# Optimization experiments

Measured on AMD Instinct MI355X. Metric: run time of the kernel, lower is better.

Reference implementation:

```python
import jax, jax.numpy as jnp
import numpy as np

B, S, D, H, G, K = 4, 4096, 1024, 16, 4, 3
DG = D // G   # group channels = 256
DH = D // H   # head channels = 64


def setup_inputs() -> dict:
    key = jax.random.key(0)
    ks = jax.random.split(key, 8)
    def w(k, shape, std=0.02):
        return jax.random.normal(k, shape, jnp.float32) * std
    return {
        "x": jax.random.normal(ks[0], (B, S, D), jnp.float32),
        "Wq": w(ks[1], (D, D)), "bq": jnp.zeros((D,), jnp.float32),
        "Wk": w(ks[2], (D, D)), "bk": jnp.zeros((D,), jnp.float32),
        "Wv": w(ks[3], (D, D)), "bv": jnp.zeros((D,), jnp.float32),
        "Wo": w(ks[4], (D, D)), "bo": jnp.zeros((D,), jnp.float32),
        "Woff1": w(ks[5], (DG, DG, K)), "boff1": jnp.zeros((DG,), jnp.float32),
        "Woff2": w(ks[6], (DG,)),
        "bias_table": w(ks[7], (1, 1, S)),
    }


def reference(x, Wq, bq, Wk, bk, Wv, bv, Wo, bo, Woff1, boff1, Woff2, bias_table):
    bsz, seq, d = x.shape
    scale = d ** (-0.5)
    xc = jnp.transpose(x, (0, 2, 1))  # [B, D, S]

    # 1x1 conv projections == channel GEMMs
    q = jnp.einsum('oc,bcs->bos', Wq, xc) + bq[None, :, None]  # [B, D, S]

    # group: [B*G, DG, S]
    gq = q.reshape(bsz * G, DG, seq)
    # offset head: conv1d(k=3, pad=1) -> conv1d(k=1, no bias) -> [B*G, S]
    h = jax.lax.conv_general_dilated(
        gq, Woff1, window_strides=(1,), padding=((K // 2, K // 2),),
        dimension_numbers=('NCH', 'OIH', 'NCH')) + boff1[None, :, None]
    offset = jnp.einsum('c,bcs->bs', Woff2, h)
    offset = jnp.tanh(offset) * K  # offset_range_factor = kernel

    gx = xc.reshape(bsz * G, DG, seq)  # grouped x

    # faithful replication of _grid_sample_1d: F.grid_sample on feats [N,C,S,1]
    # with grid (x = vgrid_scaled -> width dim of size 1, y = 0 -> height dim of
    # size S), bilinear, zero padding, align_corners=False.
    grid = jnp.arange(seq, dtype=x.dtype)[None, :]
    vgrid_scaled = 2.0 * (grid + offset) / max(seq - 1, 1) - 1.0  # [B*G, S]
    ix = vgrid_scaled / 2.0                 # unnormalized width coord (W=1)
    wx = jnp.clip(1.0 - jnp.abs(ix), 0.0, 1.0)  # bilinear weight on width idx 0
    iy = (seq - 1) / 2.0                    # unnormalized height coord for y=0
    y0 = int(np.floor(iy)); y1 = min(y0 + 1, seq - 1)
    wy1 = float(iy - y0); wy0 = 1.0 - wy1
    feat_c = wy0 * gx[:, :, y0] + wy1 * gx[:, :, y1]  # [B*G, DG]
    x_sampled = feat_c[:, :, None] * wx[:, None, :]   # [B*G, DG, S]
    xs = x_sampled.reshape(bsz, d, seq)               # ungroup -> [B, D, S]

    k = jnp.einsum('oc,bcs->bos', Wk, xs) + bk[None, :, None]
    v = jnp.einsum('oc,bcs->bos', Wv, xs) + bv[None, :, None]

    qh = q.reshape(bsz * H, DH, seq)
    kh = k.reshape(bsz * H, DH, seq)
    vh = v.reshape(bsz * H, DH, seq) + bias_table[:, :, :seq]

    # channel attention: contract over sequence dim (as in the original einsum)
    scores = jnp.einsum('bis,bjs->bij', qh, kh) * scale  # [B*H, DH, DH]
    attn = jax.nn.softmax(scores, axis=-1)
    out = jnp.einsum('bij,bjs->bis', attn, vh)           # [B*H, DH, S]
    out = out.reshape(bsz, d, seq).transpose(0, 2, 1)     # [B, S, D]
    return jnp.einsum('bsd,od->bso', out, Wo) + bo
```

## Files before the change

kernel.cpp:

```cpp
#include <hip/hip_runtime.h>
#include <math.h>

#define BB 4
#define SS 4096
#define DD 1024
#define HH 16
#define GG 4
#define KK 3
#define DG 256
#define DH 64
#define CH 16
#define NCH (SS / CH)

enum : size_t {
  OFF_WEFF  = 0,
  OFF_OFFC  = 1024,
  OFF_WEQ   = 1280,
  OFF_ZT    = 13568,
  OFF_WX    = 210176,
  OFF_XWP   = 275712,
  OFF_XW    = 5518592,
  OFF_XS    = 5534976,
  OFF_SW    = 5539072,
  OFF_FEAT  = 5539328,
  OFF_KF    = 5543424,
  OFF_VF    = 5559808,
  OFF_AV    = 5576192,
  OFF_AB    = 5592576,
  OFF_C2    = 5596672,
  OFF_WAV   = 5600768,
  OFF_WOSUM = 5617152,
  WS_FLOATS = 5618176
};

__device__ __forceinline__ float wred_sum(float v) {
#pragma unroll
  for (int o = 32; o > 0; o >>= 1) v += __shfl_xor(v, o, 64);
  return v;
}
__device__ __forceinline__ float wred_max(float v) {
#pragma unroll
  for (int o = 32; o > 0; o >>= 1) v = fmaxf(v, __shfl_xor(v, o, 64));
  return v;
}

__global__ void k_pre1(const float* __restrict__ Woff1, const float* __restrict__ Woff2,
                       const float* __restrict__ x, const float* __restrict__ Wo,
                       float* __restrict__ ws) {
  const int t = threadIdx.x;
  const int lane = t & 63;
  if (blockIdx.x < 192) {
    const int widx = (blockIdx.x * 256 + t) >> 6;
    const int i = widx / 3, kk = widx - 3 * i;
    float a = 0.f;
#pragma unroll
    for (int u = 0; u < 4; ++u) {
      const int cc = lane + 64 * u;
      a += Woff2[cc] * Woff1[(size_t)(cc * DG + i) * KK + kk];
    }
    a = wred_sum(a);
    if (lane == 0) ws[OFF_WEFF + widx] = a;
  } else if (blockIdx.x < 208) {
    const int gid = (blockIdx.x - 192) * 256 + t;
    const int b = gid >> 10, c = gid & 1023;
    ws[OFF_FEAT + gid] = 0.5f * (x[((size_t)b * SS + 2047) * DD + c] +
                                 x[((size_t)b * SS + 2048) * DD + c]);
  } else {
    const int o = ((blockIdx.x - 208) * 256 + t) >> 6;
    const float4* wo = (const float4*)(Wo + (size_t)o * DD);
    float v = 0.f;
#pragma unroll
    for (int it = 0; it < 4; ++it) {
      const float4 a = wo[lane + 64 * it];
      v += a.x + a.y + a.z + a.w;
    }
    v = wred_sum(v);
    if (lane == 0) ws[OFF_WOSUM + o] = v;
  }
}

__global__ void k_pre2(const float* __restrict__ Wq, const float* __restrict__ bq,
                       const float* __restrict__ Woff2, const float* __restrict__ boff1,
                       const float* __restrict__ Wk, const float* __restrict__ Wv,
                       float* __restrict__ ws) {
  const float* Weff = ws + OFF_WEFF;
  const int t = threadIdx.x;
  const int lane = t & 63;
  if (blockIdx.x < 192) {
    const int j = blockIdx.x >> 4;
    const int c0 = (blockIdx.x & 15) * 64;
    const int g = j / 3, kk = j - 3 * g;
    const int q = t >> 6;
    float a = 0.f;
#pragma unroll 4
    for (int ii = 0; ii < 64; ++ii) {
      const int i = q * 64 + ii;
      a += Weff[i * KK + kk] * Wq[(size_t)(g * DG + i) * DD + c0 + lane];
    }
    __shared__ float red[4][64];
    red[q][lane] = a;
    __syncthreads();
    if (q == 0) {
      const float v = red[0][lane] + red[1][lane] + red[2][lane] + red[3][lane];
      ws[OFF_WEQ + (size_t)j * DD + c0 + lane] = v;
    }
  } else if (blockIdx.x == 192) {
    if (t >= 64) return;
    float beff = 0.f;
#pragma unroll
    for (int u = 0; u < 4; ++u) {
      const int cc = lane + 64 * u;
      beff += Woff2[cc] * boff1[cc];
    }
    beff = wred_sum(beff);
#pragma unroll
    for (int g = 0; g < 4; ++g) {
      float a = 0.f;
#pragma unroll
      for (int u = 0; u < 4; ++u) {
        const int i = lane + 64 * u;
        a += (Weff[i * 3 + 0] + Weff[i * 3 + 1] + Weff[i * 3 + 2]) * bq[g * DG + i];
      }
      a = wred_sum(a);
      if (lane == 0) ws[OFF_OFFC + g] = a + beff;
    }
  } else {
    const int widx = (blockIdx.x - 193) * 4 + (t >> 6);
    const int g = widx >> 10, o = widx & 1023;
    const float4 ak = ((const float4*)(Wk + (size_t)o * DD + g * DG))[lane];
    const float4 avv = ((const float4*)(Wv + (size_t)o * DD + g * DG))[lane];
    float kk[4], vv[4];
#pragma unroll
    for (int b = 0; b < 4; ++b) {
      const float4 f = ((const float4*)(ws + OFF_FEAT + (size_t)b * DD + g * DG))[lane];
      kk[b] = ak.x * f.x + ak.y * f.y + ak.z * f.z + ak.w * f.w;
      vv[b] = avv.x * f.x + avv.y * f.y + avv.z * f.z + avv.w * f.w;
    }
#pragma unroll
    for (int b = 0; b < 4; ++b) { kk[b] = wred_sum(kk[b]); vv[b] = wred_sum(vv[b]); }
    if (lane == 0) {
#pragma unroll
      for (int b = 0; b < 4; ++b) {
        ws[OFF_KF + ((size_t)(b * GG + g)) * DD + o] = kk[b];
        ws[OFF_VF + ((size_t)(b * GG + g)) * DD + o] = vv[b];
      }
    }
  }
}

__global__ __launch_bounds__(256, 2) void k_z(const float* __restrict__ x,
                                              const float* __restrict__ weq,
                                              float* __restrict__ zt) {
  const int lane = threadIdx.x & 63;
  const int wave = (blockIdx.x * blockDim.x + threadIdx.x) >> 6;
  const int nwaves = (gridDim.x * blockDim.x) >> 6;
  float4 w[12][4];
#pragma unroll
  for (int j = 0; j < 12; ++j)
#pragma unroll
    for (int it = 0; it < 4; ++it)
      w[j][it] = *(const float4*)(weq + (size_t)j * DD + 4 * (lane + 64 * it));
  for (int row = wave; row < BB * SS; row += nwaves) {
    const float4* xr = (const float4*)(x + (size_t)row * DD);
    float4 xv[4];
#pragma unroll
    for (int it = 0; it < 4; ++it) xv[it] = xr[lane + 64 * it];
    float acc[12];
#pragma unroll
    for (int j = 0; j < 12; ++j) {
      float a = 0.f;
#pragma unroll
      for (int it = 0; it < 4; ++it)
        a += xv[it].x * w[j][it].x + xv[it].y * w[j][it].y +
             xv[it].z * w[j][it].z + xv[it].w * w[j][it].w;
      acc[j] = a;
    }
#pragma unroll
    for (int j = 0; j < 12; ++j) acc[j] = wred_sum(acc[j]);
    if (lane == 0) {
#pragma unroll
      for (int j = 0; j < 12; ++j) zt[(size_t)row * 12 + j] = acc[j];
    }
  }
}

__global__ __launch_bounds__(256) void k_xw(const float* __restrict__ x,
                                            float* __restrict__ ws) {
  const int b = blockIdx.x >> 8;
  const int chunk = blockIdx.x & 255;
  const int s0 = chunk * CH;
  const int t = threadIdx.x;
  __shared__ float wxs[4][CH];

  if (t < 64) {
    const int g = t >> 4, si = t & 15;
    const int s = s0 + si;
    const size_t row = (size_t)b * SS + s;
    const float* zt = ws + OFF_ZT;
    float off = ws[OFF_OFFC + g];
    if (s > 0)      off += zt[(row - 1) * 12 + g * 3 + 0];
    off += zt[row * 12 + g * 3 + 1];
    if (s < SS - 1) off += zt[(row + 1) * 12 + g * 3 + 2];
    off = tanhf(off) * (float)KK;
    const float vg = 2.0f * ((float)s + off) / (float)(SS - 1) - 1.0f;
    float wvv = 1.0f - fabsf(0.5f * vg);
    wvv = fminf(fmaxf(wvv, 0.0f), 1.0f);
    wxs[g][si] = wvv;
    ws[OFF_WX + (size_t)(b * GG + g) * SS + s] = wvv;
  }
  __syncthreads();

  float4 aw[5] = {};
#pragma unroll 4
  for (int si = 0; si < CH; ++si) {
    const int s = s0 + si;
    const float4 f = *(const float4*)(x + (size_t)(b * SS + s) * DD + 4 * t);
    const float w0 = wxs[0][si], w1 = wxs[1][si], w2 = wxs[2][si], w3 = wxs[3][si];
    aw[0].x += f.x * w0; aw[0].y += f.y * w0; aw[0].z += f.z * w0; aw[0].w += f.w * w0;
    aw[1].x += f.x * w1; aw[1].y += f.y * w1; aw[1].z += f.z * w1; aw[1].w += f.w * w1;
    aw[2].x += f.x * w2; aw[2].y += f.y * w2; aw[2].z += f.z * w2; aw[2].w += f.w * w2;
    aw[3].x += f.x * w3; aw[3].y += f.y * w3; aw[3].z += f.z * w3; aw[3].w += f.w * w3;
    aw[4].x += f.x; aw[4].y += f.y; aw[4].z += f.z; aw[4].w += f.w;
  }
#pragma unroll
  for (int slot = 0; slot < 5; ++slot)
    *(float4*)(ws + OFF_XWP + (((size_t)(b * 5 + slot) * NCH + chunk) * DD) + 4 * t) = aw[slot];
}

__global__ void k_red(float* __restrict__ ws) {
  const int t = threadIdx.x;
  const int lane = t & 63;
  const int wvid = t >> 6;
  __shared__ float red[4][64];
  if (blockIdx.x < 320) {
    const int rb = blockIdx.x / 80;
    const int rem = blockIdx.x - rb * 80;
    const int slot = rem >> 4;
    const int c = (rem & 15) * 64 + lane;
    const float* base = ws + OFF_XWP + (size_t)(rb * 5 + slot) * NCH * DD;
    float a = 0.f;
#pragma unroll 8
    for (int ii = 0; ii < 64; ++ii)
      a += base[(size_t)(wvid * 64 + ii) * DD + c];
    red[wvid][lane] = a;
    __syncthreads();
    if (wvid == 0) {
      const float v = red[0][lane] + red[1][lane] + red[2][lane] + red[3][lane];
      if (slot < 4) ws[OFF_XW + ((size_t)(rb * GG + slot)) * DD + c] = v;
      else          ws[OFF_XS + (size_t)rb * DD + c] = v;
    }
  } else {
    const int w = blockIdx.x - 320;
    const float* wx = ws + OFF_WX + (size_t)w * SS;
    float a = 0.f;
#pragma unroll 4
    for (int it = 0; it < 16; ++it) a += wx[t + 256 * it];
    a = wred_sum(a);
    if (lane == 0) red[0][wvid] = a;
    __syncthreads();
    if (t == 0) ws[OFF_SW + w] = red[0][0] + red[0][1] + red[0][2] + red[0][3];
  }
}

__global__ void k_mid(const float* __restrict__ Wq, const float* __restrict__ bq,
                      const float* __restrict__ bk, const float* __restrict__ bv,
                      float* __restrict__ ws) {
  const int t = threadIdx.x;
  const int lane = t & 63;
  const int wave = blockIdx.x * 4 + (t >> 6);
  const int ab_ = wave >> 10, I = wave & 1023;
  const float4* wq = (const float4*)(Wq + (size_t)I * DD);
  float4 a[4];
#pragma unroll
  for (int it = 0; it < 4; ++it) a[it] = wq[lane + 64 * it];
  float acc[5] = {0.f, 0.f, 0.f, 0.f, 0.f};
#pragma unroll
  for (int g = 0; g < 4; ++g) {
    const float4* xw = (const float4*)(ws + OFF_XW + (size_t)(ab_ * GG + g) * DD);
#pragma unroll
    for (int it = 0; it < 4; ++it) {
      const float4 c = xw[lane + 64 * it];
      acc[g] += a[it].x * c.x + a[it].y * c.y + a[it].z * c.z + a[it].w * c.w;
    }
  }
  const float4* xs = (const float4*)(ws + OFF_XS + (size_t)ab_ * DD);
#pragma unroll
  for (int it = 0; it < 4; ++it) {
    const float4 c = xs[lane + 64 * it];
    acc[4] += a[it].x * c.x + a[it].y * c.y + a[it].z * c.z + a[it].w * c.w;
  }
#pragma unroll
  for (int u = 0; u < 5; ++u) acc[u] = wred_sum(acc[u]);
  const float bqi = bq[I];
  const float q0 = acc[0] + bqi * ws[OFF_SW + ab_ * GG + 0];
  const float q1 = acc[1] + bqi * ws[OFF_SW + ab_ * GG + 1];
  const float q2 = acc[2] + bqi * ws[OFF_SW + ab_ * GG + 2];
  const float q3 = acc[3] + bqi * ws[OFF_SW + ab_ * GG + 3];
  const float qs = acc[4] + (float)SS * bqi;
  const int J = (I & ~63) | lane;
  const float* Kf = ws + OFF_KF + (size_t)ab_ * GG * DD;
  float sc = q0 * Kf[0 * DD + J] + q1 * Kf[1 * DD + J] +
             q2 * Kf[2 * DD + J] + q3 * Kf[3 * DD + J] + bk[J] * qs;
  sc *= 0.03125f;
  const float m = wred_max(sc);
  const float e = expf(sc - m);
  const float sum = wred_sum(e);
  const float attn = e / sum;
  const float* Vf = ws + OFF_VF + (size_t)ab_ * GG * DD;
#pragma unroll
  for (int g = 0; g < 4; ++g) {
    const float av = wred_sum(attn * Vf[(size_t)g * DD + J]);
    if (lane == 0) ws[OFF_AV + (size_t)wave * 4 + g] = av;
  }
  const float abv = wred_sum(attn * bv[J]);
  if (lane == 0) ws[OFF_AB + wave] = abv;
}

__global__ void k_wav(const float* __restrict__ Wo, const float* __restrict__ bo,
                      float* __restrict__ ws) {
  const int gid = blockIdx.x * blockDim.x + threadIdx.x;
  const int lane = gid & 63;
  const int w = gid >> 6;
  if (w >= BB * DD) return;
  const int b = w >> 10, o = w & 1023;
  float acc0 = 0, acc1 = 0, acc2 = 0, acc3 = 0, acc4 = 0;
  const float4* wo4 = (const float4*)(Wo + (size_t)o * DD);
  const float* AV = ws + OFF_AV + (size_t)b * DD * 4;
  const float* Ab = ws + OFF_AB + (size_t)b * DD;
#pragma unroll
  for (int it = 0; it < 4; ++it) {
    const int d4 = lane + 64 * it;
    const float4 wv = wo4[d4];
    const float4 a0 = *(const float4*)(AV + (size_t)(4 * d4 + 0) * 4);
    const float4 a1 = *(const float4*)(AV + (size_t)(4 * d4 + 1) * 4);
    const float4 a2 = *(const float4*)(AV + (size_t)(4 * d4 + 2) * 4);
    const float4 a3 = *(const float4*)(AV + (size_t)(4 * d4 + 3) * 4);
    acc0 += wv.x * a0.x + wv.y * a1.x + wv.z * a2.x + wv.w * a3.x;
    acc1 += wv.x * a0.y + wv.y * a1.y + wv.z * a2.y + wv.w * a3.y;
    acc2 += wv.x * a0.z + wv.y * a1.z + wv.z * a2.z + wv.w * a3.z;
    acc3 += wv.x * a0.w + wv.y * a1.w + wv.z * a2.w + wv.w * a3.w;
    const float4 abv = *(const float4*)(Ab + 4 * d4);
    acc4 += wv.x * abv.x + wv.y * abv.y + wv.z * abv.z + wv.w * abv.w;
  }
  acc0 = wred_sum(acc0); acc1 = wred_sum(acc1); acc2 = wred_sum(acc2);
  acc3 = wred_sum(acc3); acc4 = wred_sum(acc4);
  if (lane == 0) {
    float* WAV = ws + OFF_WAV + (size_t)w * 4;
    WAV[0] = acc0; WAV[1] = acc1; WAV[2] = acc2; WAV[3] = acc3;
    ws[OFF_C2 + w] = acc4 + bo[o];
  }
}

__global__ __launch_bounds__(256) void k_out(const float* __restrict__ btab,
                                             const float* __restrict__ ws,
                                             float* __restrict__ out) {
  const int b = blockIdx.x >> 8;
  const int ch = blockIdx.x & 255;
  const int t = threadIdx.x;
  const int o0 = 4 * t;
  float4 wav[4];
#pragma unroll
  for (int io = 0; io < 4; ++io)
    wav[io] = *(const float4*)(ws + OFF_WAV + (size_t)(b * DD + o0 + io) * 4);
  const float4 c24 = *(const float4*)(ws + OFF_C2 + (size_t)b * DD + o0);
  const float4 wos4 = *(const float4*)(ws + OFF_WOSUM + o0);
  const float* wx = ws + OFF_WX;
  const int s0 = ch * CH;
#pragma unroll 2
  for (int si = 0; si < CH; ++si) {
    const int s = s0 + si;
    const float w0 = wx[(size_t)(b * GG + 0) * SS + s];
    const float w1 = wx[(size_t)(b * GG + 1) * SS + s];
    const float w2 = wx[(size_t)(b * GG + 2) * SS + s];
    const float w3 = wx[(size_t)(b * GG + 3) * SS + s];
    const float bt = btab[s];
    float4 val;
    val.x = c24.x + bt * wos4.x + w0 * wav[0].x + w1 * wav[0].y + w2 * wav[0].z + w3 * wav[0].w;
    val.y = c24.y + bt * wos4.y + w0 * wav[1].x + w1 * wav[1].y + w2 * wav[1].z + w3 * wav[1].w;
    val.z = c24.z + bt * wos4.z + w0 * wav[2].x + w1 * wav[2].y + w2 * wav[2].z + w3 * wav[2].w;
    val.w = c24.w + bt * wos4.w + w0 * wav[3].x + w1 * wav[3].y + w2 * wav[3].z + w3 * wav[3].w;
    *(float4*)(out + (size_t)(b * SS + s) * DD + o0) = val;
  }
}

extern "C" void kernel_launch(void* const* d_in, const int* in_sizes, int n_in,
                              void* d_out, int out_size, void* d_ws, size_t ws_size,
                              hipStream_t stream) {
  const float* x     = (const float*)d_in[0];
  const float* Wq    = (const float*)d_in[1];
  const float* bq    = (const float*)d_in[2];
  const float* Wk    = (const float*)d_in[3];
  const float* bk    = (const float*)d_in[4];
  const float* Wv    = (const float*)d_in[5];
  const float* bv    = (const float*)d_in[6];
  const float* Wo    = (const float*)d_in[7];
  const float* bo    = (const float*)d_in[8];
  const float* Woff1 = (const float*)d_in[9];
  const float* boff1 = (const float*)d_in[10];
  const float* Woff2 = (const float*)d_in[11];
  const float* btab  = (const float*)d_in[12];
  float* ws  = (float*)d_ws;
  float* out = (float*)d_out;

  k_pre1<<<464, 256, 0, stream>>>(Woff1, Woff2, x, Wo, ws);
  k_pre2<<<1217, 256, 0, stream>>>(Wq, bq, Woff2, boff1, Wk, Wv, ws);
  k_z<<<512, 256, 0, stream>>>(x, ws + OFF_WEQ, ws + OFF_ZT);
  k_xw<<<1024, 256, 0, stream>>>(x, ws);
  k_red<<<336, 256, 0, stream>>>(ws);
  k_mid<<<1024, 256, 0, stream>>>(Wq, bq, bk, bv, ws);
  k_wav<<<1024, 256, 0, stream>>>(Wo, bo, ws);
  k_out<<<1024, 256, 0, stream>>>(btab, ws, out);
}
```

Before: 213.1 us.

## Fuse eight stage kernels into one persistent kernel with grid barriers

Replaces the eight separate kernel launches with one persistent kernel of 512 blocks, plus a tiny init kernel that resets the barrier counters. The stages are separated by atomic-counter global barriers, and each stage loops over its original virtual block indices. This is meant to remove per-launch overhead and the gaps between dependent kernels. In exchange it relies on all 512 blocks being co-resident to avoid deadlock, and later stages run with fewer blocks than before.

```diff
diff --git a/kernel.cpp b/kernel.cpp
--- a/kernel.cpp
+++ b/kernel.cpp
@@ -11,10 +11,12 @@
 #define DH 64
 #define CH 16
 #define NCH (SS / CH)
+#define GRID 512
 
 enum : size_t {
   OFF_WEFF  = 0,
   OFF_OFFC  = 1024,
+  OFF_BAR   = 1040,
   OFF_WEQ   = 1280,
   OFF_ZT    = 13568,
   OFF_WX    = 210176,
@@ -44,342 +46,364 @@
   return v;
 }
 
-__global__ void k_pre1(const float* __restrict__ Woff1, const float* __restrict__ Woff2,
-                       const float* __restrict__ x, const float* __restrict__ Wo,
-                       float* __restrict__ ws) {
-  const int t = threadIdx.x;
-  const int lane = t & 63;
-  if (blockIdx.x < 192) {
-    const int widx = (blockIdx.x * 256 + t) >> 6;
-    const int i = widx / 3, kk = widx - 3 * i;
-    float a = 0.f;
-#pragma unroll
-    for (int u = 0; u < 4; ++u) {
-      const int cc = lane + 64 * u;
-      a += Woff2[cc] * Woff1[(size_t)(cc * DG + i) * KK + kk];
-    }
-    a = wred_sum(a);
-    if (lane == 0) ws[OFF_WEFF + widx] = a;
-  } else if (blockIdx.x < 208) {
-    const int gid = (blockIdx.x - 192) * 256 + t;
-    const int b = gid >> 10, c = gid & 1023;
-    ws[OFF_FEAT + gid] = 0.5f * (x[((size_t)b * SS + 2047) * DD + c] +
-                                 x[((size_t)b * SS + 2048) * DD + c]);
-  } else {
-    const int o = ((blockIdx.x - 208) * 256 + t) >> 6;
-    const float4* wo = (const float4*)(Wo + (size_t)o * DD);
-    float v = 0.f;
-#pragma unroll
-    for (int it = 0; it < 4; ++it) {
-      const float4 a = wo[lane + 64 * it];
-      v += a.x + a.y + a.z + a.w;
-    }
-    v = wred_sum(v);
-    if (lane == 0) ws[OFF_WOSUM + o] = v;
-  }
-}
-
-__global__ void k_pre2(const float* __restrict__ Wq, const float* __restrict__ bq,
-                       const float* __restrict__ Woff2, const float* __restrict__ boff1,
-                       const float* __restrict__ Wk, const float* __restrict__ Wv,
-                       float* __restrict__ ws) {
-  const float* Weff = ws + OFF_WEFF;
-  const int t = threadIdx.x;
-  const int lane = t & 63;
-  if (blockIdx.x < 192) {
-    const int j = blockIdx.x >> 4;
-    const int c0 = (blockIdx.x & 15) * 64;
-    const int g = j / 3, kk = j - 3 * g;
-    const int q = t >> 6;
-    float a = 0.f;
-#pragma unroll 4
-    for (int ii = 0; ii < 64; ++ii) {
-      const int i = q * 64 + ii;
-      a += Weff[i * KK + kk] * Wq[(size_t)(g * DG + i) * DD + c0 + lane];
-    }
-    __shared__ float red[4][64];
-    red[q][lane] = a;
-    __syncthreads();
-    if (q == 0) {
-      const float v = red[0][lane] + red[1][lane] + red[2][lane] + red[3][lane];
-      ws[OFF_WEQ + (size_t)j * DD + c0 + lane] = v;
-    }
-  } else if (blockIdx.x == 192) {
-    if (t >= 64) return;
-    float beff = 0.f;
-#pragma unroll
-    for (int u = 0; u < 4; ++u) {
-      const int cc = lane + 64 * u;
-      beff += Woff2[cc] * boff1[cc];
-    }
-    beff = wred_sum(beff);
-#pragma unroll
-    for (int g = 0; g < 4; ++g) {
-      float a = 0.f;
-#pragma unroll
-      for (int u = 0; u < 4; ++u) {
-        const int i = lane + 64 * u;
-        a += (Weff[i * 3 + 0] + Weff[i * 3 + 1] + Weff[i * 3 + 2]) * bq[g * DG + i];
-      }
-      a = wred_sum(a);
-      if (lane == 0) ws[OFF_OFFC + g] = a + beff;
-    }
-  } else {
-    const int widx = (blockIdx.x - 193) * 4 + (t >> 6);
-    const int g = widx >> 10, o = widx & 1023;
-    const float4 ak = ((const float4*)(Wk + (size_t)o * DD + g * DG))[lane];
-    const float4 avv = ((const float4*)(Wv + (size_t)o * DD + g * DG))[lane];
-    float kk[4], vv[4];
-#pragma unroll
-    for (int b = 0; b < 4; ++b) {
-      const float4 f = ((const float4*)(ws + OFF_FEAT + (size_t)b * DD + g * DG))[lane];
-      kk[b] = ak.x * f.x + ak.y * f.y + ak.z * f.z + ak.w * f.w;
-      vv[b] = avv.x * f.x + avv.y * f.y + avv.z * f.z + avv.w * f.w;
-    }
-#pragma unroll
-    for (int b = 0; b < 4; ++b) { kk[b] = wred_sum(kk[b]); vv[b] = wred_sum(vv[b]); }
-    if (lane == 0) {
-#pragma unroll
-      for (int b = 0; b < 4; ++b) {
-        ws[OFF_KF + ((size_t)(b * GG + g)) * DD + o] = kk[b];
-        ws[OFF_VF + ((size_t)(b * GG + g)) * DD + o] = vv[b];
-      }
-    }
-  }
-}
-
-__global__ __launch_bounds__(256, 2) void k_z(const float* __restrict__ x,
-                                              const float* __restrict__ weq,
-                                              float* __restrict__ zt) {
-  const int lane = threadIdx.x & 63;
-  const int wave = (blockIdx.x * blockDim.x + threadIdx.x) >> 6;
-  const int nwaves = (gridDim.x * blockDim.x) >> 6;
-  float4 w[12][4];
-#pragma unroll
-  for (int j = 0; j < 12; ++j)
-#pragma unroll
-    for (int it = 0; it < 4; ++it)
-      w[j][it] = *(const float4*)(weq + (size_t)j * DD + 4 * (lane + 64 * it));
-  for (int row = wave; row < BB * SS; row += nwaves) {
-    const float4* xr = (const float4*)(x + (size_t)row * DD);
-    float4 xv[4];
-#pragma unroll
-    for (int it = 0; it < 4; ++it) xv[it] = xr[lane + 64 * it];
-    float acc[12];
-#pragma unroll
-    for (int j = 0; j < 12; ++j) {
-      float a = 0.f;
-#pragma unroll
-      for (int it = 0; it < 4; ++it)
-        a += xv[it].x * w[j][it].x + xv[it].y * w[j][it].y +
-             xv[it].z * w[j][it].z + xv[it].w * w[j][it].w;
-      acc[j] = a;
-    }
-#pragma unroll
-    for (int j = 0; j < 12; ++j) acc[j] = wred_sum(acc[j]);
-    if (lane == 0) {
-#pragma unroll
-      for (int j = 0; j < 12; ++j) zt[(size_t)row * 12 + j] = acc[j];
-    }
-  }
-}
-
-__global__ __launch_bounds__(256) void k_xw(const float* __restrict__ x,
-                                            float* __restrict__ ws) {
-  const int b = blockIdx.x >> 8;
-  const int chunk = blockIdx.x & 255;
-  const int s0 = chunk * CH;
-  const int t = threadIdx.x;
-  __shared__ float wxs[4][CH];
-
-  if (t < 64) {
-    const int g = t >> 4, si = t & 15;
-    const int s = s0 + si;
-    const size_t row = (size_t)b * SS + s;
-    const float* zt = ws + OFF_ZT;
-    float off = ws[OFF_OFFC + g];
-    if (s > 0)      off += zt[(row - 1) * 12 + g * 3 + 0];
-    off += zt[row * 12 + g * 3 + 1];
-    if (s < SS - 1) off += zt[(row + 1) * 12 + g * 3 + 2];
-    off = tanhf(off) * (float)KK;
-    const float vg = 2.0f * ((float)s + off) / (float)(SS - 1) - 1.0f;
-    float wvv = 1.0f - fabsf(0.5f * vg);
-    wvv = fminf(fmaxf(wvv, 0.0f), 1.0f);
-    wxs[g][si] = wvv;
-    ws[OFF_WX + (size_t)(b * GG + g) * SS + s] = wvv;
-  }
+__global__ void k_init(float* __restrict__ ws) {
+  if (threadIdx.x < 2) ((unsigned*)(ws + OFF_BAR))[threadIdx.x] = 0u;
+}
+
+__device__ __forceinline__ void gbar(unsigned* bar, unsigned tgt) {
   __syncthreads();
-
-  float4 aw[5] = {};
-#pragma unroll 4
-  for (int si = 0; si < CH; ++si) {
-    const int s = s0 + si;
-    const float4 f = *(const float4*)(x + (size_t)(b * SS + s) * DD + 4 * t);
-    const float w0 = wxs[0][si], w1 = wxs[1][si], w2 = wxs[2][si], w3 = wxs[3][si];
-    aw[0].x += f.x * w0; aw[0].y += f.y * w0; aw[0].z += f.z * w0; aw[0].w += f.w * w0;
-    aw[1].x += f.x * w1; aw[1].y += f.y * w1; aw[1].z += f.z * w1; aw[1].w += f.w * w1;
-    aw[2].x += f.x * w2; aw[2].y += f.y * w2; aw[2].z += f.z * w2; aw[2].w += f.w * w2;
-    aw[3].x += f.x * w3; aw[3].y += f.y * w3; aw[3].z += f.z * w3; aw[3].w += f.w * w3;
-    aw[4].x += f.x; aw[4].y += f.y; aw[4].z += f.z; aw[4].w += f.w;
-  }
-#pragma unroll
-  for (int slot = 0; slot < 5; ++slot)
-    *(float4*)(ws + OFF_XWP + (((size_t)(b * 5 + slot) * NCH + chunk) * DD) + 4 * t) = aw[slot];
-}
-
-__global__ void k_red(float* __restrict__ ws) {
+  if (threadIdx.x == 0) {
+    __threadfence();
+    const unsigned prev = atomicAdd(&bar[0], 1u);
+    if (prev == (unsigned)(GRID - 1)) {
+      atomicExch(&bar[0], 0u);
+      __threadfence();
+      atomicAdd(&bar[1], 1u);
+    } else {
+      while (__hip_atomic_load(&bar[1], __ATOMIC_RELAXED, __HIP_MEMORY_SCOPE_AGENT) < tgt) {
+        __builtin_amdgcn_s_sleep(8);
+      }
+    }
+    __threadfence();
+  }
+  __syncthreads();
+}
+
+extern "C" __global__ __launch_bounds__(256, 2) void k_mega(
+    const float* __restrict__ x,  const float* __restrict__ Wq, const float* __restrict__ bq,
+    const float* __restrict__ Wk, const float* __restrict__ bk,
+    const float* __restrict__ Wv, const float* __restrict__ bv,
+    const float* __restrict__ Wo, const float* __restrict__ bo,
+    const float* __restrict__ Woff1, const float* __restrict__ boff1,
+    const float* __restrict__ Woff2, const float* __restrict__ btab,
+    float* __restrict__ ws, float* __restrict__ out) {
   const int t = threadIdx.x;
   const int lane = t & 63;
   const int wvid = t >> 6;
-  __shared__ float red[4][64];
-  if (blockIdx.x < 320) {
-    const int rb = blockIdx.x / 80;
-    const int rem = blockIdx.x - rb * 80;
-    const int slot = rem >> 4;
-    const int c = (rem & 15) * 64 + lane;
-    const float* base = ws + OFF_XWP + (size_t)(rb * 5 + slot) * NCH * DD;
-    float a = 0.f;
+  const int bid = blockIdx.x;
+  unsigned* bar = (unsigned*)(ws + OFF_BAR);
+  unsigned bg = 0;
+  __shared__ float smem[256];
+
+  for (int vb = bid; vb < 464; vb += GRID) {
+    if (vb < 192) {
+      const int widx = (vb * 256 + t) >> 6;
+      const int i = widx / 3, kk = widx - 3 * i;
+      float a = 0.f;
+#pragma unroll
+      for (int u = 0; u < 4; ++u) {
+        const int cc = lane + 64 * u;
+        a += Woff2[cc] * Woff1[(size_t)(cc * DG + i) * KK + kk];
+      }
+      a = wred_sum(a);
+      if (lane == 0) ws[OFF_WEFF + widx] = a;
+    } else if (vb < 208) {
+      const int gid = (vb - 192) * 256 + t;
+      const int b = gid >> 10, c = gid & 1023;
+      ws[OFF_FEAT + gid] = 0.5f * (x[((size_t)b * SS + 2047) * DD + c] +
+                                   x[((size_t)b * SS + 2048) * DD + c]);
+    } else {
+      const int o = ((vb - 208) * 256 + t) >> 6;
+      const float4* wo = (const float4*)(Wo + (size_t)o * DD);
+      float v = 0.f;
+#pragma unroll
+      for (int it = 0; it < 4; ++it) {
+        const float4 a = wo[lane + 64 * it];
+        v += a.x + a.y + a.z + a.w;
+      }
+      v = wred_sum(v);
+      if (lane == 0) ws[OFF_WOSUM + o] = v;
+    }
+  }
+  gbar(bar, ++bg);
+
+  {
+    const float* Weff = ws + OFF_WEFF;
+    for (int vb = bid; vb < 1217; vb += GRID) {
+      __syncthreads();
+      if (vb < 192) {
+        const int j = vb >> 4;
+        const int c0 = (vb & 15) * 64;
+        const int g = j / 3, kk = j - 3 * g;
+        const int q = t >> 6;
+        float a = 0.f;
+#pragma unroll 4
+        for (int ii = 0; ii < 64; ++ii) {
+          const int i = q * 64 + ii;
+          a += Weff[i * KK + kk] * Wq[(size_t)(g * DG + i) * DD + c0 + lane];
+        }
+        smem[q * 64 + lane] = a;
+        __syncthreads();
+        if (q == 0) {
+          const float v = smem[lane] + smem[64 + lane] + smem[128 + lane] + smem[192 + lane];
+          ws[OFF_WEQ + (size_t)j * DD + c0 + lane] = v;
+        }
+      } else if (vb == 192) {
+        if (t < 64) {
+          float beff = 0.f;
+#pragma unroll
+          for (int u = 0; u < 4; ++u) {
+            const int cc = lane + 64 * u;
+            beff += Woff2[cc] * boff1[cc];
+          }
+          beff = wred_sum(beff);
+#pragma unroll
+          for (int g = 0; g < 4; ++g) {
+            float a = 0.f;
+#pragma unroll
+            for (int u = 0; u < 4; ++u) {
+              const int i = lane + 64 * u;
+              a += (Weff[i * 3 + 0] + Weff[i * 3 + 1] + Weff[i * 3 + 2]) * bq[g * DG + i];
+            }
+            a = wred_sum(a);
+            if (lane == 0) ws[OFF_OFFC + g] = a + beff;
+          }
+        }
+      } else {
+        const int widx = (vb - 193) * 4 + (t >> 6);
+        const int g = widx >> 10, o = widx & 1023;
+        const float4 ak  = ((const float4*)(Wk + (size_t)o * DD + g * DG))[lane];
+        const float4 avv = ((const float4*)(Wv + (size_t)o * DD + g * DG))[lane];
+        float kk4[4], vv4[4];
+#pragma unroll
+        for (int b = 0; b < 4; ++b) {
+          const float4 f = ((const float4*)(ws + OFF_FEAT + (size_t)b * DD + g * DG))[lane];
+          kk4[b] = ak.x * f.x + ak.y * f.y + ak.z * f.z + ak.w * f.w;
+          vv4[b] = avv.x * f.x + avv.y * f.y + avv.z * f.z + avv.w * f.w;
+        }
+#pragma unroll
+        for (int b = 0; b < 4; ++b) { kk4[b] = wred_sum(kk4[b]); vv4[b] = wred_sum(vv4[b]); }
+        if (lane == 0) {
+#pragma unroll
+          for (int b = 0; b < 4; ++b) {
+            ws[OFF_KF + ((size_t)(b * GG + g)) * DD + o] = kk4[b];
+            ws[OFF_VF + ((size_t)(b * GG + g)) * DD + o] = vv4[b];
+          }
+        }
+      }
+    }
+  }
+  gbar(bar, ++bg);
+
+  {
+    const float* weq = ws + OFF_WEQ;
+    float* zt = ws + OFF_ZT;
+    const int wave = (bid * 256 + t) >> 6;
+    const int nwaves = (GRID * 256) >> 6;
+    float4 w[12][4];
+#pragma unroll
+    for (int j = 0; j < 12; ++j)
+#pragma unroll
+      for (int it = 0; it < 4; ++it)
+        w[j][it] = *(const float4*)(weq + (size_t)j * DD + 4 * (lane + 64 * it));
+    for (int row = wave; row < BB * SS; row += nwaves) {
+      const float4* xr = (const float4*)(x + (size_t)row * DD);
+      float4 xv[4];
+#pragma unroll
+      for (int it = 0; it < 4; ++it) xv[it] = xr[lane + 64 * it];
+      float acc[12];
+#pragma unroll
+      for (int j = 0; j < 12; ++j) {
+        float a = 0.f;
+#pragma unroll
+        for (int it = 0; it < 4; ++it)
+          a += xv[it].x * w[j][it].x + xv[it].y * w[j][it].y +
+               xv[it].z * w[j][it].z + xv[it].w * w[j][it].w;
+        acc[j] = a;
+      }
+#pragma unroll
+      for (int j = 0; j < 12; ++j) acc[j] = wred_sum(acc[j]);
+      if (lane == 0) {
+#pragma unroll
+        for (int j = 0; j < 12; ++j) zt[(size_t)row * 12 + j] = acc[j];
+      }
+    }
+  }
+  gbar(bar, ++bg);
+
+  for (int vb = bid; vb < BB * NCH; vb += GRID) {
+    const int b = vb >> 8;
+    const int chunk = vb & 255;
+    const int s0 = chunk * CH;
+    __syncthreads();
+    if (t < 64) {
+      const int g = t >> 4, si = t & 15;
+      const int s = s0 + si;
+      const size_t row = (size_t)b * SS + s;
+      const float* zt = ws + OFF_ZT;
+      float off = ws[OFF_OFFC + g];
+      if (s > 0)      off += zt[(row - 1) * 12 + g * 3 + 0];
+      off += zt[row * 12 + g * 3 + 1];
+      if (s < SS - 1) off += zt[(row + 1) * 12 + g * 3 + 2];
+      off = tanhf(off) * (float)KK;
+      const float vg = 2.0f * ((float)s + off) / (float)(SS - 1) - 1.0f;
+      float wvv = 1.0f - fabsf(0.5f * vg);
+      wvv = fminf(fmaxf(wvv, 0.0f), 1.0f);
+      smem[t] = wvv;
+      ws[OFF_WX + (size_t)(b * GG + g) * SS + s] = wvv;
+    }
+    __syncthreads();
+    float4 aw[5] = {};
+#pragma unroll 4
+    for (int si = 0; si < CH; ++si) {
+      const int s = s0 + si;
+      const float4 f = *(const float4*)(x + (size_t)(b * SS + s) * DD + 4 * t);
+      const float w0 = smem[si], w1 = smem[16 + si], w2 = smem[32 + si], w3 = smem[48 + si];
+      aw[0].x += f.x * w0; aw[0].y += f.y * w0; aw[0].z += f.z * w0; aw[0].w += f.w * w0;
+      aw[1].x += f.x * w1; aw[1].y += f.y * w1; aw[1].z += f.z * w1; aw[1].w += f.w * w1;
+      aw[2].x += f.x * w2; aw[2].y += f.y * w2; aw[2].z += f.z * w2; aw[2].w += f.w * w2;
+      aw[3].x += f.x * w3; aw[3].y += f.y * w3; aw[3].z += f.z * w3; aw[3].w += f.w * w3;
+      aw[4].x += f.x; aw[4].y += f.y; aw[4].z += f.z; aw[4].w += f.w;
+    }
+#pragma unroll
+    for (int slot = 0; slot < 5; ++slot)
+      *(float4*)(ws + OFF_XWP + (((size_t)(b * 5 + slot) * NCH + chunk) * DD) + 4 * t) = aw[slot];
+  }
+  gbar(bar, ++bg);
+
+  for (int vb = bid; vb < 336; vb += GRID) {
+    __syncthreads();
+    if (vb < 320) {
+      const int rb = vb / 80;
+      const int rem = vb - rb * 80;
+      const int slot = rem >> 4;
+      const int c = (rem & 15) * 64 + lane;
+      const float* base = ws + OFF_XWP + (size_t)(rb * 5 + slot) * NCH * DD;
+      float a = 0.f;
 #pragma unroll 8
-    for (int ii = 0; ii < 64; ++ii)
-      a += base[(size_t)(wvid * 64 + ii) * DD + c];
-    red[wvid][lane] = a;
-    __syncthreads();
-    if (wvid == 0) {
-      const float v = red[0][lane] + red[1][lane] + red[2][lane] + red[3][lane];
-      if (slot < 4) ws[OFF_XW + ((size_t)(rb * GG + slot)) * DD + c] = v;
-      else          ws[OFF_XS + (size_t)rb * DD + c] = v;
-    }
-  } else {
-    const int w = blockIdx.x - 320;
-    const float* wx = ws + OFF_WX + (size_t)w * SS;
-    float a = 0.f;
+      for (int ii = 0; ii < 64; ++ii)
+        a += base[(size_t)(wvid * 64 + ii) * DD + c];
+      smem[wvid * 64 + lane] = a;
+      __syncthreads();
+      if (wvid == 0) {
+        const float v = smem[lane] + smem[64 + lane] + smem[128 + lane] + smem[192 + lane];
+        if (slot < 4) ws[OFF_XW + ((size_t)(rb * GG + slot)) * DD + c] = v;
+        else          ws[OFF_XS + (size_t)rb * DD + c] = v;
+      }
+    } else {
+      const int w = vb - 320;
+      const float* wx = ws + OFF_WX + (size_t)w * SS;
+      float a = 0.f;
 #pragma unroll 4
-    for (int it = 0; it < 16; ++it) a += wx[t + 256 * it];
-    a = wred_sum(a);
-    if (lane == 0) red[0][wvid] = a;
-    __syncthreads();
-    if (t == 0) ws[OFF_SW + w] = red[0][0] + red[0][1] + red[0][2] + red[0][3];
-  }
-}
-
-__global__ void k_mid(const float* __restrict__ Wq, const float* __restrict__ bq,
-                      const float* __restrict__ bk, const float* __restrict__ bv,
-                      float* __restrict__ ws) {
-  const int t = threadIdx.x;
-  const int lane = t & 63;
-  const int wave = blockIdx.x * 4 + (t >> 6);
-  const int ab_ = wave >> 10, I = wave & 1023;
-  const float4* wq = (const float4*)(Wq + (size_t)I * DD);
-  float4 a[4];
-#pragma unroll
-  for (int it = 0; it < 4; ++it) a[it] = wq[lane + 64 * it];
-  float acc[5] = {0.f, 0.f, 0.f, 0.f, 0.f};
-#pragma unroll
-  for (int g = 0; g < 4; ++g) {
-    const float4* xw = (const float4*)(ws + OFF_XW + (size_t)(ab_ * GG + g) * DD);
+      for (int it = 0; it < 16; ++it) a += wx[t + 256 * it];
+      a = wred_sum(a);
+      if (lane == 0) smem[wvid] = a;
+      __syncthreads();
+      if (t == 0) ws[OFF_SW + w] = smem[0] + smem[1] + smem[2] + smem[3];
+    }
+  }
+  gbar(bar, ++bg);
+
+  for (int vb = bid; vb < 1024; vb += GRID) {
+    const int wave = vb * 4 + wvid;
+    const int ab_ = wave >> 10, I = wave & 1023;
+    const float4* wq = (const float4*)(Wq + (size_t)I * DD);
+    float4 a[4];
+#pragma unroll
+    for (int it = 0; it < 4; ++it) a[it] = wq[lane + 64 * it];
+    float acc[5] = {0.f, 0.f, 0.f, 0.f, 0.f};
+#pragma unroll
+    for (int g = 0; g < 4; ++g) {
+      const float4* xw = (const float4*)(ws + OFF_XW + (size_t)(ab_ * GG + g) * DD);
+#pragma unroll
+      for (int it = 0; it < 4; ++it) {
+        const float4 c = xw[lane + 64 * it];
+        acc[g] += a[it].x * c.x + a[it].y * c.y + a[it].z * c.z + a[it].w * c.w;
+      }
+    }
+    const float4* xs = (const float4*)(ws + OFF_XS + (size_t)ab_ * DD);
 #pragma unroll
     for (int it = 0; it < 4; ++it) {
-      const float4 c = xw[lane + 64 * it];
-      acc[g] += a[it].x * c.x + a[it].y * c.y + a[it].z * c.z + a[it].w * c.w;
-    }
-  }
-  const float4* xs = (const float4*)(ws + OFF_XS + (size_t)ab_ * DD);
-#pragma unroll
-  for (int it = 0; it < 4; ++it) {
-    const float4 c = xs[lane + 64 * it];
-    acc[4] += a[it].x * c.x + a[it].y * c.y + a[it].z * c.z + a[it].w * c.w;
-  }
-#pragma unroll
-  for (int u = 0; u < 5; ++u) acc[u] = wred_sum(acc[u]);
-  const float bqi = bq[I];
-  const float q0 = acc[0] + bqi * ws[OFF_SW + ab_ * GG + 0];
-  const float q1 = acc[1] + bqi * ws[OFF_SW + ab_ * GG + 1];
-  const float q2 = acc[2] + bqi * ws[OFF_SW + ab_ * GG + 2];
-  const float q3 = acc[3] + bqi * ws[OFF_SW + ab_ * GG + 3];
-  const float qs = acc[4] + (float)SS * bqi;
-  const int J = (I & ~63) | lane;
-  const float* Kf = ws + OFF_KF + (size_t)ab_ * GG * DD;
-  float sc = q0 * Kf[0 * DD + J] + q1 * Kf[1 * DD + J] +
-             q2 * Kf[2 * DD + J] + q3 * Kf[3 * DD + J] + bk[J] * qs;
-  sc *= 0.03125f;
-  const float m = wred_max(sc);
-  const float e = expf(sc - m);
-  const float sum = wred_sum(e);
-  const float attn = e / sum;
-  const float* Vf = ws + OFF_VF + (size_t)ab_ * GG * DD;
-#pragma unroll
-  for (int g = 0; g < 4; ++g) {
-    const float av = wred_sum(attn * Vf[(size_t)g * DD + J]);
-    if (lane == 0) ws[OFF_AV + (size_t)wave * 4 + g] = av;
-  }
-  const float abv = wred_sum(attn * bv[J]);
-  if (lane == 0) ws[OFF_AB + wave] = abv;
-}
-
-__global__ void k_wav(const float* __restrict__ Wo, const float* __restrict__ bo,
-                      float* __restrict__ ws) {
-  const int gid = blockIdx.x * blockDim.x + threadIdx.x;
-  const int lane = gid & 63;
-  const int w = gid >> 6;
-  if (w >= BB * DD) return;
-  const int b = w >> 10, o = w & 1023;
-  float acc0 = 0, acc1 = 0, acc2 = 0, acc3 = 0, acc4 = 0;
-  const float4* wo4 = (const float4*)(Wo + (size_t)o * DD);
-  const float* AV = ws + OFF_AV + (size_t)b * DD * 4;
-  const float* Ab = ws + OFF_AB + (size_t)b * DD;
-#pragma unroll
-  for (int it = 0; it < 4; ++it) {
-    const int d4 = lane + 64 * it;
-    const float4 wv = wo4[d4];
-    const float4 a0 = *(const float4*)(AV + (size_t)(4 * d4 + 0) * 4);
-    const float4 a1 = *(const float4*)(AV + (size_t)(4 * d4 + 1) * 4);
-    const float4 a2 = *(const float4*)(AV + (size_t)(4 * d4 + 2) * 4);
-    const float4 a3 = *(const float4*)(AV + (size_t)(4 * d4 + 3) * 4);
-    acc0 += wv.x * a0.x + wv.y * a1.x + wv.z * a2.x + wv.w * a3.x;
-    acc1 += wv.x * a0.y + wv.y * a1.y + wv.z * a2.y + wv.w * a3.y;
-    acc2 += wv.x * a0.z + wv.y * a1.z + wv.z * a2.z + wv.w * a3.z;
-    acc3 += wv.x * a0.w + wv.y * a1.w + wv.z * a2.w + wv.w * a3.w;
-    const float4 abv = *(const float4*)(Ab + 4 * d4);
-    acc4 += wv.x * abv.x + wv.y * abv.y + wv.z * abv.z + wv.w * abv.w;
-  }
-  acc0 = wred_sum(acc0); acc1 = wred_sum(acc1); acc2 = wred_sum(acc2);
-  acc3 = wred_sum(acc3); acc4 = wred_sum(acc4);
-  if (lane == 0) {
-    float* WAV = ws + OFF_WAV + (size_t)w * 4;
-    WAV[0] = acc0; WAV[1] = acc1; WAV[2] = acc2; WAV[3] = acc3;
-    ws[OFF_C2 + w] = acc4 + bo[o];
-  }
-}
-
-__global__ __launch_bounds__(256) void k_out(const float* __restrict__ btab,
-                                             const float* __restrict__ ws,
-                                             float* __restrict__ out) {
-  const int b = blockIdx.x >> 8;
-  const int ch = blockIdx.x & 255;
-  const int t = threadIdx.x;
-  const int o0 = 4 * t;
-  float4 wav[4];
-#pragma unroll
-  for (int io = 0; io < 4; ++io)
-    wav[io] = *(const float4*)(ws + OFF_WAV + (size_t)(b * DD + o0 + io) * 4);
-  const float4 c24 = *(const float4*)(ws + OFF_C2 + (size_t)b * DD + o0);
-  const float4 wos4 = *(const float4*)(ws + OFF_WOSUM + o0);
-  const float* wx = ws + OFF_WX;
-  const int s0 = ch * CH;
+      const float4 c = xs[lane + 64 * it];
+      acc[4] += a[it].x * c.x + a[it].y * c.y + a[it].z * c.z + a[it].w * c.w;
+    }
+#pragma unroll
+    for (int u = 0; u < 5; ++u) acc[u] = wred_sum(acc[u]);
+    const float bqi = bq[I];
+    const float q0 = acc[0] + bqi * ws[OFF_SW + ab_ * GG + 0];
+    const float q1 = acc[1] + bqi * ws[OFF_SW + ab_ * GG + 1];
+    const float q2 = acc[2] + bqi * ws[OFF_SW + ab_ * GG + 2];
+    const float q3 = acc[3] + bqi * ws[OFF_SW + ab_ * GG + 3];
+    const float qs = acc[4] + (float)SS * bqi;
+    const int J = (I & ~63) | lane;
+    const float* Kf = ws + OFF_KF + (size_t)ab_ * GG * DD;
+    float sc = q0 * Kf[0 * DD + J] + q1 * Kf[1 * DD + J] +
+               q2 * Kf[2 * DD + J] + q3 * Kf[3 * DD + J] + bk[J] * qs;
+    sc *= 0.03125f;
+    const float m = wred_max(sc);
+    const float e = expf(sc - m);
+    const float sum = wred_sum(e);
+    const float attn = e / sum;
+    const float* Vf = ws + OFF_VF + (size_t)ab_ * GG * DD;
+#pragma unroll
+    for (int g = 0; g < 4; ++g) {
+      const float av = wred_sum(attn * Vf[(size_t)g * DD + J]);
+      if (lane == 0) ws[OFF_AV + (size_t)wave * 4 + g] = av;
+    }
+    const float abv = wred_sum(attn * bv[J]);
+    if (lane == 0) ws[OFF_AB + wave] = abv;
+  }
+  gbar(bar, ++bg);
+
+  for (int vb = bid; vb < 1024; vb += GRID) {
+    const int w = vb * 4 + wvid;
+    const int b = w >> 10, o = w & 1023;
+    float acc0 = 0, acc1 = 0, acc2 = 0, acc3 = 0, acc4 = 0;
+    const float4* wo4 = (const float4*)(Wo + (size_t)o * DD);
+    const float* AV = ws + OFF_AV + (size_t)b * DD * 4;
+    const float* Ab = ws + OFF_AB + (size_t)b * DD;
+#pragma unroll
+    for (int it = 0; it < 4; ++it) {
+      const int d4 = lane + 64 * it;
+      const float4 wv4 = wo4[d4];
+      const float4 a0 = *(const float4*)(AV + (size_t)(4 * d4 + 0) * 4);
+      const float4 a1 = *(const float4*)(AV + (size_t)(4 * d4 + 1) * 4);
+      const float4 a2 = *(const float4*)(AV + (size_t)(4 * d4 + 2) * 4);
+      const float4 a3 = *(const float4*)(AV + (size_t)(4 * d4 + 3) * 4);
+      acc0 += wv4.x * a0.x + wv4.y * a1.x + wv4.z * a2.x + wv4.w * a3.x;
+      acc1 += wv4.x * a0.y + wv4.y * a1.y + wv4.z * a2.y + wv4.w * a3.y;
+      acc2 += wv4.x * a0.z + wv4.y * a1.z + wv4.z * a2.z + wv4.w * a3.z;
+      acc3 += wv4.x * a0.w + wv4.y * a1.w + wv4.z * a2.w + wv4.w * a3.w;
+      const float4 abv = *(const float4*)(Ab + 4 * d4);
+      acc4 += wv4.x * abv.x + wv4.y * abv.y + wv4.z * abv.z + wv4.w * abv.w;
+    }
+    acc0 = wred_sum(acc0); acc1 = wred_sum(acc1); acc2 = wred_sum(acc2);
+    acc3 = wred_sum(acc3); acc4 = wred_sum(acc4);
+    if (lane == 0) {
+      float* WAV = ws + OFF_WAV + (size_t)w * 4;
+      WAV[0] = acc0; WAV[1] = acc1; WAV[2] = acc2; WAV[3] = acc3;
+      ws[OFF_C2 + w] = acc4 + bo[o];
+    }
+  }
+  gbar(bar, ++bg);
+
+  for (int vb = bid; vb < 1024; vb += GRID) {
+    const int b = vb >> 8;
+    const int ch = vb & 255;
+    const int o0 = 4 * t;
+    float4 wav[4];
+#pragma unroll
+    for (int io = 0; io < 4; ++io)
+      wav[io] = *(const float4*)(ws + OFF_WAV + (size_t)(b * DD + o0 + io) * 4);
+    const float4 c24  = *(const float4*)(ws + OFF_C2 + (size_t)b * DD + o0);
+    const float4 wos4 = *(const float4*)(ws + OFF_WOSUM + o0);
+    const float* wx = ws + OFF_WX;
+    const int s0 = ch * CH;
 #pragma unroll 2
-  for (int si = 0; si < CH; ++si) {
-    const int s = s0 + si;
-    const float w0 = wx[(size_t)(b * GG + 0) * SS + s];
-    const float w1 = wx[(size_t)(b * GG + 1) * SS + s];
-    const float w2 = wx[(size_t)(b * GG + 2) * SS + s];
-    const float w3 = wx[(size_t)(b * GG + 3) * SS + s];
-    const float bt = btab[s];
-    float4 val;
-    val.x = c24.x + bt * wos4.x + w0 * wav[0].x + w1 * wav[0].y + w2 * wav[0].z + w3 * wav[0].w;
-    val.y = c24.y + bt * wos4.y + w0 * wav[1].x + w1 * wav[1].y + w2 * wav[1].z + w3 * wav[1].w;
-    val.z = c24.z + bt * wos4.z + w0 * wav[2].x + w1 * wav[2].y + w2 * wav[2].z + w3 * wav[2].w;
-    val.w = c24.w + bt * wos4.w + w0 * wav[3].x + w1 * wav[3].y + w2 * wav[3].z + w3 * wav[3].w;
-    *(float4*)(out + (size_t)(b * SS + s) * DD + o0) = val;
+    for (int si = 0; si < CH; ++si) {
+      const int s = s0 + si;
+      const float w0 = wx[(size_t)(b * GG + 0) * SS + s];
+      const float w1 = wx[(size_t)(b * GG + 1) * SS + s];
+      const float w2 = wx[(size_t)(b * GG + 2) * SS + s];
+      const float w3 = wx[(size_t)(b * GG + 3) * SS + s];
+      const float bt = btab[s];
+      float4 val;
+      val.x = c24.x + bt * wos4.x + w0 * wav[0].x + w1 * wav[0].y + w2 * wav[0].z + w3 * wav[0].w;
+      val.y = c24.y + bt * wos4.y + w0 * wav[1].x + w1 * wav[1].y + w2 * wav[1].z + w3 * wav[1].w;
+      val.z = c24.z + bt * wos4.z + w0 * wav[2].x + w1 * wav[2].y + w2 * wav[2].z + w3 * wav[2].w;
+      val.w = c24.w + bt * wos4.w + w0 * wav[3].x + w1 * wav[3].y + w2 * wav[3].z + w3 * wav[3].w;
+      *(float4*)(out + (size_t)(b * SS + s) * DD + o0) = val;
+    }
   }
 }
 
@@ -400,14 +424,9 @@
   const float* Woff2 = (const float*)d_in[11];
   const float* btab  = (const float*)d_in[12];
   float* ws  = (float*)d_ws;
-  float* out = (float*)d_out;
-
-  k_pre1<<<464, 256, 0, stream>>>(Woff1, Woff2, x, Wo, ws);
-  k_pre2<<<1217, 256, 0, stream>>>(Wq, bq, Woff2, boff1, Wk, Wv, ws);
-  k_z<<<512, 256, 0, stream>>>(x, ws + OFF_WEQ, ws + OFF_ZT);
-  k_xw<<<1024, 256, 0, stream>>>(x, ws);
-  k_red<<<336, 256, 0, stream>>>(ws);
-  k_mid<<<1024, 256, 0, stream>>>(Wq, bq, bk, bv, ws);
-  k_wav<<<1024, 256, 0, stream>>>(Wo, bo, ws);
-  k_out<<<1024, 256, 0, stream>>>(btab, ws, out);
-}
+  float* outp = (float*)d_out;
+
+  k_init<<<1, 64, 0, stream>>>(ws);
+  k_mega<<<GRID, 256, 0, stream>>>(x, Wq, bq, Wk, bk, Wv, bv, Wo, bo,
+                                   Woff1, boff1, Woff2, btab, ws, outp);
+}
```

Result: slower. 572.0 us (+168.4%).
